# Kernel tuning notes

Measured on AMD Instinct MI355X. Metric: run time of the kernel, lower is better.

## Reference

```python
import jax, jax.numpy as jnp
import numpy as np

B, D = 4096, 512
INIT_TEMP = 0.07
TEMP_MAX = 100.0


def setup_inputs() -> dict:
    key = jax.random.key(0)
    k1, k2, k3, k4 = jax.random.split(key, 4)
    return {
        "v_mean": jax.random.normal(k1, (B, D), dtype=jnp.float32),
        "v_var": jax.random.uniform(k2, (B, D), dtype=jnp.float32),
        "t_mean": jax.random.normal(k3, (B, D), dtype=jnp.float32),
        "t_var": jax.random.uniform(k4, (B, D), dtype=jnp.float32),
        "log_temp": jnp.log(jnp.asarray(1.0 / INIT_TEMP, dtype=jnp.float32)),
    }


def _pairwise_sq_dist(a, b):
    # ||a_i - b_j||^2 = ||a_i||^2 + ||b_j||^2 - 2 a_i . b_j  (GEMM expansion)
    a_sq = jnp.sum(a * a, axis=-1)            # [B]
    b_sq = jnp.sum(b * b, axis=-1)            # [B]
    cross = jnp.einsum('id,jd->ij', a, b)     # [B, B] GEMM
    return a_sq[:, None] + b_sq[None, :] - 2.0 * cross


def reference(v_mean, v_var, t_mean, t_var, log_temp):
    temperature = jnp.minimum(jnp.exp(log_temp), TEMP_MAX)
    v_sigma = jnp.sqrt(v_var)
    t_sigma = jnp.sqrt(t_var)
    # W2^2 between diagonal Gaussians (as in source: term1 + term2 only)
    w2 = _pairwise_sq_dist(v_mean, t_mean) + _pairwise_sq_dist(v_sigma, t_sigma)
    logits = -w2 * temperature                # [B, B]
    n = logits.shape[0]
    diag = jnp.arange(n)
    # CE(logits, arange): rows for image->text, columns for text->image
    logp_i = jax.nn.log_softmax(logits, axis=1)
    logp_t = jax.nn.log_softmax(logits, axis=0)
    loss_i = -jnp.mean(logp_i[diag, diag])
    loss_t = -jnp.mean(logp_t[diag, diag])
    return (loss_i + loss_t) * 0.5
```

## Files before the change

kernel.cpp:

```cpp
#include <hip/hip_runtime.h>
#include <math.h>

#define NB 4096
#define ND 512
#define K2 1024
#define NT16 16

typedef __attribute__((ext_vector_type(16))) float f32x16;

__global__ __launch_bounds__(256) void prep_kernel(
    const float* __restrict__ v_mean, const float* __restrict__ v_var,
    const float* __restrict__ t_mean, const float* __restrict__ t_var,
    unsigned char* __restrict__ Afp, unsigned char* __restrict__ Bfp,
    float* __restrict__ a_sq, float* __restrict__ b_sq) {
  __shared__ __align__(8) unsigned char lfp[32 * 132];
  int bid = blockIdx.x;
  int tid = threadIdx.x;
  const float* src;
  unsigned char* dst;
  float* sq;
  int row0;
  bool isVar;
  if (bid < 1024) {
    int rb = bid >> 5, t = (bid >> 2) & 7, g = bid & 3;
    row0 = rb * 128 + g * 32;
    isVar = t >= 4;
    src = (isVar ? v_var : v_mean) + (size_t)row0 * ND + (t & 3) * 128;
    dst = Afp + (size_t)rb * 131072 + t * 16384 + g * 4096;
    sq = a_sq;
  } else {
    int b = bid - 1024;
    int rb = b >> 6, t = (b >> 3) & 7, g = b & 7;
    row0 = rb * 256 + g * 32;
    isVar = t >= 4;
    src = (isVar ? t_var : t_mean) + (size_t)row0 * ND + (t & 3) * 128;
    dst = Bfp + (size_t)rb * 262144 + t * 32768 + g * 4096;
    sq = b_sq;
  }
#pragma unroll
  for (int q = 0; q < 4; ++q) {
    int flat = q * 256 + tid;
    int row = flat >> 5, col4 = flat & 31;
    float4 v = *(const float4*)(src + row * ND + col4 * 4);
    float p;
    float4 w;
    if (isVar) {
      p = (v.x + v.y) + (v.z + v.w);
      w.x = sqrtf(v.x); w.y = sqrtf(v.y); w.z = sqrtf(v.z); w.w = sqrtf(v.w);
    } else {
      p = (v.x * v.x + v.y * v.y) + (v.z * v.z + v.w * v.w);
      w = v;
    }
    int p01 = __builtin_amdgcn_cvt_pk_fp8_f32(w.x, w.y, 0, false);
    int p23 = __builtin_amdgcn_cvt_pk_fp8_f32(w.z, w.w, 0, false);
    unsigned u = (unsigned)(p01 & 0xFFFF) | ((unsigned)(p23 & 0xFFFF) << 16);
    *(unsigned*)(lfp + row * 132 + col4 * 4) = u;
#pragma unroll
    for (int o = 1; o <= 16; o <<= 1) p += __shfl_xor(p, o);
    if ((tid & 31) == 0) atomicAdd(sq + row0 + row, p);
  }
  __syncthreads();
  {
    int wv = tid >> 6, l = tid & 63;
    int r5 = l & 31, kh = l >> 5;
#pragma unroll
    for (int cc = 0; cc < 2; ++cc) {
      int ks8 = wv * 2 + cc;
      unsigned long long d =
          *(const unsigned long long*)(lfp + r5 * 132 + ks8 * 16 + kh * 8);
      *(unsigned long long*)(dst + ks8 * 512 + l * 8) = d;
    }
  }
}

__global__ __launch_bounds__(512, 4) void gemm_fused_kernel(
    const unsigned char* __restrict__ Afp, const unsigned char* __restrict__ Bfp,
    const float* __restrict__ a_sq, const float* __restrict__ b_sq,
    const float* __restrict__ log_temp,
    float* __restrict__ rowM, float* __restrict__ rowS,
    float* __restrict__ colM, float* __restrict__ colS,
    float* __restrict__ diag) {
  __shared__ unsigned char ldsA[2][8192];
  __shared__ unsigned char ldsB[2][16384];
  int bid = blockIdx.x;
  int swz = (bid & 7) * 64 + (bid >> 3);
  int bm = swz >> 4, bn = swz & 15;
  int brow = bm * 128, bcol = bn * 256;
  int tid = threadIdx.x;
  int lane = tid & 63, wid = tid >> 6;
  int wr = wid >> 2, wc = wid & 3;
  int l31 = lane & 31, kh = lane >> 5;

  const unsigned char* Ablk = Afp + (size_t)bm * 131072;
  const unsigned char* Bblk = Bfp + (size_t)bn * 262144;

  int gA = tid >> 7;
  unsigned offA = (unsigned)(tid & 127) * 16;

#define STAGE(TT, C)                                                           \
  {                                                                            \
    unsigned t16 = (unsigned)((TT) >> 1) * 16384u;                             \
    unsigned t32 = (unsigned)((TT) >> 1) * 32768u;                             \
    unsigned hf = (unsigned)((TT) & 1) * 2048u;                                \
    __builtin_amdgcn_global_load_lds(                                          \
        (const __attribute__((address_space(1))) unsigned int*)(Ablk + t16 +   \
            gA * 4096 + hf + offA),                                            \
        (__attribute__((address_space(3))) unsigned int*)(&ldsA[C][0] +        \
            gA * 2048 + offA),                                                 \
        16, 0, 0);                                                             \
    _Pragma("unroll") for (int cc = 0; cc < 2; ++cc)                           \
        __builtin_amdgcn_global_load_lds(                                      \
            (const __attribute__((address_space(1))) unsigned int*)(Bblk +     \
                t32 + (cc * 4 + gA) * 4096 + hf + offA),                       \
            (__attribute__((address_space(3))) unsigned int*)(&ldsB[C][0] +    \
                (cc * 4 + gA) * 2048 + offA),                                  \
            16, 0, 0);                                                         \
  }

  unsigned aB0 = (unsigned)(wr * 2 + 0) * 2048 + lane * 8;
  unsigned aB1 = (unsigned)(wr * 2 + 1) * 2048 + lane * 8;
  unsigned bB0 = (unsigned)(wc * 2 + 0) * 2048 + lane * 8;
  unsigned bB1 = (unsigned)(wc * 2 + 1) * 2048 + lane * 8;

  f32x16 acc[2][2] = {};

  STAGE(0, 0);
  asm volatile("s_waitcnt vmcnt(0)" ::: "memory");
  __builtin_amdgcn_s_barrier();

  for (int tt = 0; tt < NT16; ++tt) {
    const int c = tt & 1;
    const unsigned char* bufa = &ldsA[c][0];
    const unsigned char* bufb = &ldsB[c][0];
    if (tt + 1 < NT16) STAGE(tt + 1, c ^ 1);
#pragma unroll
    for (int ks = 0; ks < 4; ++ks) {
      unsigned ko = (unsigned)ks * 512;
      long a0 = *(const long*)(bufa + aB0 + ko);
      long a1 = *(const long*)(bufa + aB1 + ko);
      long b0 = *(const long*)(bufb + bB0 + ko);
      long b1 = *(const long*)(bufb + bB1 + ko);
      __builtin_amdgcn_s_setprio(1);
      acc[0][0] = __builtin_amdgcn_mfma_f32_32x32x16_fp8_fp8(a0, b0, acc[0][0], 0, 0, 0);
      acc[0][1] = __builtin_amdgcn_mfma_f32_32x32x16_fp8_fp8(a0, b1, acc[0][1], 0, 0, 0);
      acc[1][0] = __builtin_amdgcn_mfma_f32_32x32x16_fp8_fp8(a1, b0, acc[1][0], 0, 0, 0);
      acc[1][1] = __builtin_amdgcn_mfma_f32_32x32x16_fp8_fp8(a1, b1, acc[1][1], 0, 0, 0);
      __builtin_amdgcn_s_setprio(0);
    }
    asm volatile("s_waitcnt lgkmcnt(0)" ::: "memory");
    asm volatile("s_waitcnt vmcnt(0)" ::: "memory");
    __builtin_amdgcn_s_barrier();
  }

  float temp = fminf(expf(log_temp[0]), 100.0f);
#pragma unroll
  for (int mi = 0; mi < 2; ++mi) {
#pragma unroll
    for (int reg = 0; reg < 16; ++reg) {
      int rl = wr * 64 + mi * 32 + (reg & 3) + 8 * (reg >> 2) + 4 * kh;
      float asq = a_sq[brow + rl];
#pragma unroll
      for (int ni = 0; ni < 2; ++ni) {
        float bsq = b_sq[bcol + wc * 64 + ni * 32 + l31];
        acc[mi][ni][reg] = -temp * (asq + bsq - 2.0f * acc[mi][ni][reg]);
      }
    }
  }
  if ((bm >> 1) == bn) {
#pragma unroll
    for (int mi = 0; mi < 2; ++mi)
#pragma unroll
      for (int ni = 0; ni < 2; ++ni)
#pragma unroll
        for (int reg = 0; reg < 16; ++reg) {
          int rl = wr * 64 + mi * 32 + (reg & 3) + 8 * (reg >> 2) + 4 * kh;
          int cl = wc * 64 + ni * 32 + l31;
          if (brow + rl == bcol + cl) diag[brow + rl] = acc[mi][ni][reg];
        }
  }
#pragma unroll
  for (int mi = 0; mi < 2; ++mi) {
#pragma unroll
    for (int reg = 0; reg < 16; ++reg) {
      float mx = fmaxf(acc[mi][0][reg], acc[mi][1][reg]);
#pragma unroll
      for (int o = 1; o < 32; o <<= 1) mx = fmaxf(mx, __shfl_xor(mx, o));
      float s = __expf(acc[mi][0][reg] - mx) + __expf(acc[mi][1][reg] - mx);
#pragma unroll
      for (int o = 1; o < 32; o <<= 1) s += __shfl_xor(s, o);
      if (l31 == 0) {
        int row = brow + wr * 64 + mi * 32 + (reg & 3) + 8 * (reg >> 2) + 4 * kh;
        int ch = bn * 4 + wc;
        rowM[(size_t)row * 64 + ch] = mx;
        rowS[(size_t)row * 64 + ch] = s;
      }
    }
  }
#pragma unroll
  for (int ni = 0; ni < 2; ++ni) {
    float mx = -INFINITY;
#pragma unroll
    for (int mi = 0; mi < 2; ++mi)
#pragma unroll
      for (int reg = 0; reg < 16; ++reg) mx = fmaxf(mx, acc[mi][ni][reg]);
    mx = fmaxf(mx, __shfl_xor(mx, 32));
    float s = 0.f;
#pragma unroll
    for (int mi = 0; mi < 2; ++mi)
#pragma unroll
      for (int reg = 0; reg < 16; ++reg) s += __expf(acc[mi][ni][reg] - mx);
    s += __shfl_xor(s, 32);
    if (kh == 0) {
      int col = bcol + wc * 64 + ni * 32 + l31;
      int ch = bm * 2 + wr;
      colM[(size_t)col * 64 + ch] = mx;
      colS[(size_t)col * 64 + ch] = s;
    }
  }
}

__global__ __launch_bounds__(256) void combine_kernel(
    const float* __restrict__ rowM, const float* __restrict__ rowS,
    const float* __restrict__ colM, const float* __restrict__ colS,
    const float* __restrict__ diag, float* __restrict__ hrow,
    float* __restrict__ hcol) {
  int b = blockIdx.x;
  int t = threadIdx.x;
  int wave = t >> 6, lane = t & 63;
  int isCol = b >> 10;
  int idx = (b & 1023) * 4 + wave;
  const float* PM = isCol ? colM : rowM;
  const float* PS = isCol ? colS : rowS;
  float M = PM[(size_t)idx * 64 + lane];
  float S = PS[(size_t)idx * 64 + lane];
#pragma unroll
  for (int o = 1; o < 64; o <<= 1) {
    float M2 = __shfl_xor(M, o), S2 = __shfl_xor(S, o);
    float nM = fmaxf(M, M2);
    S = S * __expf(M - nM) + S2 * __expf(M2 - nM);
    M = nM;
  }
  if (lane == 0) {
    float v = M + logf(S) - diag[idx];
    (isCol ? hcol : hrow)[idx] = v;
  }
}

__global__ __launch_bounds__(256) void final_kernel(
    const float* __restrict__ hrow, const float* __restrict__ hcol,
    float* __restrict__ out) {
  int t = threadIdx.x;
  double a = 0.0;
  for (int i = t; i < NB; i += 256) {
    a += 0.5 * ((double)hrow[i] + (double)hcol[i]);
  }
#pragma unroll
  for (int o = 32; o > 0; o >>= 1) a += __shfl_xor(a, o);
  __shared__ double sd[4];
  if ((t & 63) == 0) sd[t >> 6] = a;
  __syncthreads();
  if (t == 0) out[0] = (float)(((sd[0] + sd[1]) + (sd[2] + sd[3])) / (double)NB);
}

extern "C" void kernel_launch(void* const* d_in, const int* in_sizes, int n_in,
                              void* d_out, int out_size, void* d_ws, size_t ws_size,
                              hipStream_t stream) {
  const float* v_mean = (const float*)d_in[0];
  const float* v_var = (const float*)d_in[1];
  const float* t_mean = (const float*)d_in[2];
  const float* t_var = (const float*)d_in[3];
  const float* log_temp = (const float*)d_in[4];
  float* out = (float*)d_out;

  char* ws = (char*)d_ws;
  unsigned char* Afp = (unsigned char*)ws;
  unsigned char* Bfp = (unsigned char*)(ws + 4194304);
  float* rowM = (float*)(ws + 8388608);
  float* rowS = rowM + (size_t)NB * 64;
  float* colM = rowS + (size_t)NB * 64;
  float* colS = colM + (size_t)NB * 64;
  float* diag = colS + (size_t)NB * 64;
  float* hrow = diag + NB;
  float* hcol = hrow + NB;
  float* a_sq = hcol + NB;
  float* b_sq = a_sq + NB;

  hipMemsetAsync(a_sq, 0, 2 * (size_t)NB * sizeof(float), stream);
  prep_kernel<<<2048, 256, 0, stream>>>(v_mean, v_var, t_mean, t_var, Afp, Bfp, a_sq, b_sq);
  gemm_fused_kernel<<<512, 512, 0, stream>>>(Afp, Bfp, a_sq, b_sq, log_temp,
                                             rowM, rowS, colM, colS, diag);
  combine_kernel<<<2048, 256, 0, stream>>>(rowM, rowS, colM, colS, diag, hrow, hcol);
  final_kernel<<<1, 256, 0, stream>>>(hrow, hcol, out);
}
```

Baseline: 69.00 us.

## Enlarge per-wave GEMM tile, single-buffer deeper K stages, and fold final reduction into atomics

The GEMM drops from 8 to 4 waves per block, with each wave computing a 64x128 tile (2x4 MFMA accumulators) instead of 64x64, for more operand reuse per LDS read. The K loop now stages 32 K-steps per tile in a single LDS buffer instead of double-buffered 16-step halves. The next stage is issued after a barrier and overlaps only the last MFMA group. The final reduction kernel is removed: combine_kernel atomically adds scaled per-row and per-column terms into the output, which prep_kernel zeroes. This saves a launch but makes the float sum order nondeterministic and less precise than the old double-precision sum, and the single buffer exposes more load latency.

```diff
diff --git a/kernel.cpp b/kernel.cpp
--- a/kernel.cpp
+++ b/kernel.cpp
@@ -4,7 +4,7 @@
 #define NB 4096
 #define ND 512
 #define K2 1024
-#define NT16 16
+#define NT8 8
 
 typedef __attribute__((ext_vector_type(16))) float f32x16;
 
@@ -12,10 +12,12 @@
     const float* __restrict__ v_mean, const float* __restrict__ v_var,
     const float* __restrict__ t_mean, const float* __restrict__ t_var,
     unsigned char* __restrict__ Afp, unsigned char* __restrict__ Bfp,
-    float* __restrict__ a_sq, float* __restrict__ b_sq) {
+    float* __restrict__ a_sq, float* __restrict__ b_sq,
+    float* __restrict__ out) {
   __shared__ __align__(8) unsigned char lfp[32 * 132];
   int bid = blockIdx.x;
   int tid = threadIdx.x;
+  if (bid == 0 && tid == 0) out[0] = 0.f;
   const float* src;
   unsigned char* dst;
   float* sq;
@@ -73,81 +75,86 @@
   }
 }
 
-__global__ __launch_bounds__(512, 4) void gemm_fused_kernel(
+__global__ __launch_bounds__(256, 2) void gemm_fused_kernel(
     const unsigned char* __restrict__ Afp, const unsigned char* __restrict__ Bfp,
     const float* __restrict__ a_sq, const float* __restrict__ b_sq,
     const float* __restrict__ log_temp,
     float* __restrict__ rowM, float* __restrict__ rowS,
     float* __restrict__ colM, float* __restrict__ colS,
     float* __restrict__ diag) {
-  __shared__ unsigned char ldsA[2][8192];
-  __shared__ unsigned char ldsB[2][16384];
+  __shared__ unsigned char ldsA[16384];
+  __shared__ unsigned char ldsB[32768];
   int bid = blockIdx.x;
   int swz = (bid & 7) * 64 + (bid >> 3);
   int bm = swz >> 4, bn = swz & 15;
   int brow = bm * 128, bcol = bn * 256;
   int tid = threadIdx.x;
   int lane = tid & 63, wid = tid >> 6;
-  int wr = wid >> 2, wc = wid & 3;
+  int wr = wid >> 1, wc = wid & 1;
   int l31 = lane & 31, kh = lane >> 5;
 
   const unsigned char* Ablk = Afp + (size_t)bm * 131072;
   const unsigned char* Bblk = Bfp + (size_t)bn * 262144;
-
-  int gA = tid >> 7;
-  unsigned offA = (unsigned)(tid & 127) * 16;
-
-#define STAGE(TT, C)                                                           \
+  unsigned off16 = (unsigned)tid * 16;
+
+#define STAGE(TT)                                                              \
   {                                                                            \
-    unsigned t16 = (unsigned)((TT) >> 1) * 16384u;                             \
-    unsigned t32 = (unsigned)((TT) >> 1) * 32768u;                             \
-    unsigned hf = (unsigned)((TT) & 1) * 2048u;                                \
-    __builtin_amdgcn_global_load_lds(                                          \
-        (const __attribute__((address_space(1))) unsigned int*)(Ablk + t16 +   \
-            gA * 4096 + hf + offA),                                            \
-        (__attribute__((address_space(3))) unsigned int*)(&ldsA[C][0] +        \
-            gA * 2048 + offA),                                                 \
-        16, 0, 0);                                                             \
-    _Pragma("unroll") for (int cc = 0; cc < 2; ++cc)                           \
+    _Pragma("unroll") for (int s = 0; s < 4; ++s)                              \
+        __builtin_amdgcn_global_load_lds(                                      \
+            (const __attribute__((address_space(1))) unsigned int*)(Ablk +     \
+                (unsigned)(TT) * 16384u + s * 4096u + off16),                  \
+            (__attribute__((address_space(3))) unsigned int*)(ldsA +           \
+                s * 4096u + off16),                                            \
+            16, 0, 0);                                                         \
+    _Pragma("unroll") for (int s = 0; s < 8; ++s)                              \
         __builtin_amdgcn_global_load_lds(                                      \
             (const __attribute__((address_space(1))) unsigned int*)(Bblk +     \
-                t32 + (cc * 4 + gA) * 4096 + hf + offA),                       \
-            (__attribute__((address_space(3))) unsigned int*)(&ldsB[C][0] +    \
-                (cc * 4 + gA) * 2048 + offA),                                  \
+                (unsigned)(TT) * 32768u + s * 4096u + off16),                  \
+            (__attribute__((address_space(3))) unsigned int*)(ldsB +           \
+                s * 4096u + off16),                                            \
             16, 0, 0);                                                         \
   }
 
-  unsigned aB0 = (unsigned)(wr * 2 + 0) * 2048 + lane * 8;
-  unsigned aB1 = (unsigned)(wr * 2 + 1) * 2048 + lane * 8;
-  unsigned bB0 = (unsigned)(wc * 2 + 0) * 2048 + lane * 8;
-  unsigned bB1 = (unsigned)(wc * 2 + 1) * 2048 + lane * 8;
-
-  f32x16 acc[2][2] = {};
-
-  STAGE(0, 0);
+  unsigned aB0 = (unsigned)(wr * 2 + 0) * 4096 + lane * 8;
+  unsigned aB1 = (unsigned)(wr * 2 + 1) * 4096 + lane * 8;
+  unsigned bBs = (unsigned)(wc * 4) * 4096 + lane * 8;
+
+  f32x16 acc[2][4] = {};
+
+  STAGE(0);
   asm volatile("s_waitcnt vmcnt(0)" ::: "memory");
   __builtin_amdgcn_s_barrier();
 
-  for (int tt = 0; tt < NT16; ++tt) {
-    const int c = tt & 1;
-    const unsigned char* bufa = &ldsA[c][0];
-    const unsigned char* bufb = &ldsB[c][0];
-    if (tt + 1 < NT16) STAGE(tt + 1, c ^ 1);
-#pragma unroll
-    for (int ks = 0; ks < 4; ++ks) {
-      unsigned ko = (unsigned)ks * 512;
-      long a0 = *(const long*)(bufa + aB0 + ko);
-      long a1 = *(const long*)(bufa + aB1 + ko);
-      long b0 = *(const long*)(bufb + bB0 + ko);
-      long b1 = *(const long*)(bufb + bB1 + ko);
-      __builtin_amdgcn_s_setprio(1);
-      acc[0][0] = __builtin_amdgcn_mfma_f32_32x32x16_fp8_fp8(a0, b0, acc[0][0], 0, 0, 0);
-      acc[0][1] = __builtin_amdgcn_mfma_f32_32x32x16_fp8_fp8(a0, b1, acc[0][1], 0, 0, 0);
-      acc[1][0] = __builtin_amdgcn_mfma_f32_32x32x16_fp8_fp8(a1, b0, acc[1][0], 0, 0, 0);
-      acc[1][1] = __builtin_amdgcn_mfma_f32_32x32x16_fp8_fp8(a1, b1, acc[1][1], 0, 0, 0);
-      __builtin_amdgcn_s_setprio(0);
-    }
+  for (int tt = 0; tt < NT8; ++tt) {
+    long a0, a1, b0, b1, b2, b3;
+#define LOADKS(KO)                                                             \
+    a0 = *(const long*)(ldsA + aB0 + (KO));                                    \
+    a1 = *(const long*)(ldsA + aB1 + (KO));                                    \
+    b0 = *(const long*)(ldsB + bBs + 0 * 4096 + (KO));                         \
+    b1 = *(const long*)(ldsB + bBs + 1 * 4096 + (KO));                         \
+    b2 = *(const long*)(ldsB + bBs + 2 * 4096 + (KO));                         \
+    b3 = *(const long*)(ldsB + bBs + 3 * 4096 + (KO));
+#define MFMA8()                                                                \
+    __builtin_amdgcn_s_setprio(1);                                             \
+    acc[0][0] = __builtin_amdgcn_mfma_f32_32x32x16_fp8_fp8(a0, b0, acc[0][0], 0, 0, 0); \
+    acc[0][1] = __builtin_amdgcn_mfma_f32_32x32x16_fp8_fp8(a0, b1, acc[0][1], 0, 0, 0); \
+    acc[0][2] = __builtin_amdgcn_mfma_f32_32x32x16_fp8_fp8(a0, b2, acc[0][2], 0, 0, 0); \
+    acc[0][3] = __builtin_amdgcn_mfma_f32_32x32x16_fp8_fp8(a0, b3, acc[0][3], 0, 0, 0); \
+    acc[1][0] = __builtin_amdgcn_mfma_f32_32x32x16_fp8_fp8(a1, b0, acc[1][0], 0, 0, 0); \
+    acc[1][1] = __builtin_amdgcn_mfma_f32_32x32x16_fp8_fp8(a1, b1, acc[1][1], 0, 0, 0); \
+    acc[1][2] = __builtin_amdgcn_mfma_f32_32x32x16_fp8_fp8(a1, b2, acc[1][2], 0, 0, 0); \
+    acc[1][3] = __builtin_amdgcn_mfma_f32_32x32x16_fp8_fp8(a1, b3, acc[1][3], 0, 0, 0); \
+    __builtin_amdgcn_s_setprio(0);
+#pragma unroll
+    for (int ks = 0; ks < 7; ++ks) {
+      LOADKS((unsigned)ks * 512)
+      MFMA8()
+    }
+    LOADKS(3584u)
     asm volatile("s_waitcnt lgkmcnt(0)" ::: "memory");
+    __builtin_amdgcn_s_barrier();
+    if (tt + 1 < NT8) STAGE(tt + 1);
+    MFMA8()
     asm volatile("s_waitcnt vmcnt(0)" ::: "memory");
     __builtin_amdgcn_s_barrier();
   }
@@ -160,8 +167,8 @@
       int rl = wr * 64 + mi * 32 + (reg & 3) + 8 * (reg >> 2) + 4 * kh;
       float asq = a_sq[brow + rl];
 #pragma unroll
-      for (int ni = 0; ni < 2; ++ni) {
-        float bsq = b_sq[bcol + wc * 64 + ni * 32 + l31];
+      for (int ni = 0; ni < 4; ++ni) {
+        float bsq = b_sq[bcol + wc * 128 + ni * 32 + l31];
         acc[mi][ni][reg] = -temp * (asq + bsq - 2.0f * acc[mi][ni][reg]);
       }
     }
@@ -170,11 +177,11 @@
 #pragma unroll
     for (int mi = 0; mi < 2; ++mi)
 #pragma unroll
-      for (int ni = 0; ni < 2; ++ni)
+      for (int ni = 0; ni < 4; ++ni)
 #pragma unroll
         for (int reg = 0; reg < 16; ++reg) {
           int rl = wr * 64 + mi * 32 + (reg & 3) + 8 * (reg >> 2) + 4 * kh;
-          int cl = wc * 64 + ni * 32 + l31;
+          int cl = wc * 128 + ni * 32 + l31;
           if (brow + rl == bcol + cl) diag[brow + rl] = acc[mi][ni][reg];
         }
   }
@@ -182,22 +189,25 @@
   for (int mi = 0; mi < 2; ++mi) {
 #pragma unroll
     for (int reg = 0; reg < 16; ++reg) {
-      float mx = fmaxf(acc[mi][0][reg], acc[mi][1][reg]);
-#pragma unroll
-      for (int o = 1; o < 32; o <<= 1) mx = fmaxf(mx, __shfl_xor(mx, o));
-      float s = __expf(acc[mi][0][reg] - mx) + __expf(acc[mi][1][reg] - mx);
-#pragma unroll
-      for (int o = 1; o < 32; o <<= 1) s += __shfl_xor(s, o);
-      if (l31 == 0) {
-        int row = brow + wr * 64 + mi * 32 + (reg & 3) + 8 * (reg >> 2) + 4 * kh;
-        int ch = bn * 4 + wc;
-        rowM[(size_t)row * 64 + ch] = mx;
-        rowS[(size_t)row * 64 + ch] = s;
+      int row = brow + wr * 64 + mi * 32 + (reg & 3) + 8 * (reg >> 2) + 4 * kh;
+#pragma unroll
+      for (int c = 0; c < 2; ++c) {
+        float mx = fmaxf(acc[mi][2 * c][reg], acc[mi][2 * c + 1][reg]);
+#pragma unroll
+        for (int o = 1; o < 32; o <<= 1) mx = fmaxf(mx, __shfl_xor(mx, o));
+        float s = __expf(acc[mi][2 * c][reg] - mx) + __expf(acc[mi][2 * c + 1][reg] - mx);
+#pragma unroll
+        for (int o = 1; o < 32; o <<= 1) s += __shfl_xor(s, o);
+        if (l31 == 0) {
+          int ch = bn * 4 + wc * 2 + c;
+          rowM[(size_t)row * 64 + ch] = mx;
+          rowS[(size_t)row * 64 + ch] = s;
+        }
       }
     }
   }
 #pragma unroll
-  for (int ni = 0; ni < 2; ++ni) {
+  for (int ni = 0; ni < 4; ++ni) {
     float mx = -INFINITY;
 #pragma unroll
     for (int mi = 0; mi < 2; ++mi)
@@ -211,7 +221,7 @@
       for (int reg = 0; reg < 16; ++reg) s += __expf(acc[mi][ni][reg] - mx);
     s += __shfl_xor(s, 32);
     if (kh == 0) {
-      int col = bcol + wc * 64 + ni * 32 + l31;
+      int col = bcol + wc * 128 + ni * 32 + l31;
       int ch = bm * 2 + wr;
       colM[(size_t)col * 64 + ch] = mx;
       colS[(size_t)col * 64 + ch] = s;
@@ -222,8 +232,7 @@
 __global__ __launch_bounds__(256) void combine_kernel(
     const float* __restrict__ rowM, const float* __restrict__ rowS,
     const float* __restrict__ colM, const float* __restrict__ colS,
-    const float* __restrict__ diag, float* __restrict__ hrow,
-    float* __restrict__ hcol) {
+    const float* __restrict__ diag, float* __restrict__ out) {
   int b = blockIdx.x;
   int t = threadIdx.x;
   int wave = t >> 6, lane = t & 63;
@@ -242,24 +251,8 @@
   }
   if (lane == 0) {
     float v = M + logf(S) - diag[idx];
-    (isCol ? hcol : hrow)[idx] = v;
-  }
-}
-
-__global__ __launch_bounds__(256) void final_kernel(
-    const float* __restrict__ hrow, const float* __restrict__ hcol,
-    float* __restrict__ out) {
-  int t = threadIdx.x;
-  double a = 0.0;
-  for (int i = t; i < NB; i += 256) {
-    a += 0.5 * ((double)hrow[i] + (double)hcol[i]);
-  }
-#pragma unroll
-  for (int o = 32; o > 0; o >>= 1) a += __shfl_xor(a, o);
-  __shared__ double sd[4];
-  if ((t & 63) == 0) sd[t >> 6] = a;
-  __syncthreads();
-  if (t == 0) out[0] = (float)(((sd[0] + sd[1]) + (sd[2] + sd[3])) / (double)NB);
+    atomicAdd(out, v * (0.5f / (float)NB));
+  }
 }
 
 extern "C" void kernel_launch(void* const* d_in, const int* in_sizes, int n_in,
@@ -280,15 +273,13 @@
   float* colM = rowS + (size_t)NB * 64;
   float* colS = colM + (size_t)NB * 64;
   float* diag = colS + (size_t)NB * 64;
-  float* hrow = diag + NB;
-  float* hcol = hrow + NB;
-  float* a_sq = hcol + NB;
+  float* a_sq = diag + NB;
   float* b_sq = a_sq + NB;
 
   hipMemsetAsync(a_sq, 0, 2 * (size_t)NB * sizeof(float), stream);
-  prep_kernel<<<2048, 256, 0, stream>>>(v_mean, v_var, t_mean, t_var, Afp, Bfp, a_sq, b_sq);
-  gemm_fused_kernel<<<512, 512, 0, stream>>>(Afp, Bfp, a_sq, b_sq, log_temp,
+  prep_kernel<<<2048, 256, 0, stream>>>(v_mean, v_var, t_mean, t_var, Afp, Bfp,
+                                        a_sq, b_sq, out);
+  gemm_fused_kernel<<<512, 256, 0, stream>>>(Afp, Bfp, a_sq, b_sq, log_temp,
                                              rowM, rowS, colM, colS, diag);
-  combine_kernel<<<2048, 256, 0, stream>>>(rowM, rowS, colM, colS, diag, hrow, hcol);
-  final_kernel<<<1, 256, 0, stream>>>(hrow, hcol, out);
-}
+  combine_kernel<<<2048, 256, 0, stream>>>(rowM, rowS, colM, colS, diag, out);
+}
```

Measured after the change: 177.2 us. 2.57x slower.
